# Kernel optimization log

Hardware: AMD Instinct MI355X
Metric: run time of the kernel (lower is better)

Reference implementation:

```python
import jax, jax.numpy as jnp
import numpy as np

HIDDEN = 4096


def setup_inputs() -> dict:
    key = jax.random.key(0)
    k1, k2 = jax.random.split(key)
    hidden_states = jax.random.normal(k1, (8, 2048, HIDDEN), dtype=jnp.float32)
    # gate_proj ~ N(0, 0.02^2), shape (2*hidden, hidden)
    gate_proj = 0.02 * jax.random.normal(k2, (2 * HIDDEN, HIDDEN), dtype=jnp.float32)
    return {"hidden_states": hidden_states, "gate_proj": gate_proj, "world_size": 8}


def reference(hidden_states, gate_proj, world_size):
    h = gate_proj.shape[1]
    view = hidden_states.reshape(-1, h)                 # [N, h]
    mm = jnp.einsum("nh,oh->no", view, gate_proj)      # [N, 2h]  (x @ W.T)
    n, o = mm.shape
    # reduce-scatter over dim 0 with world_size ranks: sum the per-rank chunks
    out = mm.reshape(world_size, n // world_size, o).sum(axis=0)  # [N/W, 2h]
    return out
```

## Files before the change

kernel.cpp:

```cpp
#include <hip/hip_runtime.h>
#include <hip/hip_bf16.h>


#define HID   4096
#define SEQ   2048
#define WORLD 8
#define OUTD  8192

typedef __bf16 bf16x8 __attribute__((ext_vector_type(8)));
typedef short  s16x8  __attribute__((ext_vector_type(8)));
typedef float  f32x4  __attribute__((ext_vector_type(4)));

typedef const __attribute__((address_space(1))) void* gas1_ptr;
typedef __attribute__((address_space(3))) void*       las3_ptr;

static __device__ __forceinline__ unsigned short f2bf(float f) {
    union { float f; unsigned u; } v; v.f = f;
    unsigned u = v.u;
    u += 0x7fffu + ((u >> 16) & 1u);
    return (unsigned short)(u >> 16);
}

#define RED_BLOCKS  2048
#define CONV_BLOCKS 4096
__global__ void prep_kernel(const float* __restrict__ hs,
                            const float* __restrict__ w,
                            unsigned short* __restrict__ xb,
                            unsigned short* __restrict__ wb) {
    if (blockIdx.x < RED_BLOCKS) {
        const int total4 = SEQ * HID / 4;
        const float4* h4 = (const float4*)hs;
        ushort4* o4 = (ushort4*)xb;
        for (int i = blockIdx.x * blockDim.x + threadIdx.x; i < total4;
             i += RED_BLOCKS * blockDim.x) {
            float4 s = h4[i];
            #pragma unroll
            for (int ww = 1; ww < WORLD; ++ww) {
                float4 t = h4[i + ww * total4];
                s.x += t.x; s.y += t.y; s.z += t.z; s.w += t.w;
            }
            ushort4 o;
            o.x = f2bf(s.x); o.y = f2bf(s.y); o.z = f2bf(s.z); o.w = f2bf(s.w);
            o4[i] = o;
        }
    } else {
        const int total4 = OUTD * HID / 4;
        const float4* w4 = (const float4*)w;
        ushort4* o4 = (ushort4*)wb;
        for (int i = (blockIdx.x - RED_BLOCKS) * blockDim.x + threadIdx.x;
             i < total4; i += CONV_BLOCKS * blockDim.x) {
            float4 s = w4[i];
            ushort4 o;
            o.x = f2bf(s.x); o.y = f2bf(s.y); o.z = f2bf(s.z); o.w = f2bf(s.w);
            o4[i] = o;
        }
    }
}


#define BM 256
#define BN 256
#define BK 64
#define KSTEPS (HID / BK)

__global__ __launch_bounds__(512, 2)
void gemm_bt_kernel(const unsigned short* __restrict__ A,
                    const unsigned short* __restrict__ B,
                    float* __restrict__ C) {
    __shared__ __align__(16) unsigned short lsA[2][BM * BK];
    __shared__ __align__(16) unsigned short lsB[2][BN * BK];

    const int tid  = threadIdx.x;
    const int lane = tid & 63;
    const int wave = tid >> 6;
    const int wm   = wave >> 2;
    const int wn   = wave & 3;

    const int bid   = blockIdx.x;
    const int xcd   = bid & 7;
    const int local = bid >> 3;
    const int bm = (xcd >> 2) * 4 + (local >> 3);
    const int bn = (xcd & 3) * 8 + (local & 7);

    const int subrow = lane >> 3;
    const int slot   = lane & 7;
    const int scol   = (slot ^ subrow) * 8;
    const unsigned short* aBase =
        A + (size_t)(bm * BM + wave * 8 + subrow) * HID + scol;
    const unsigned short* bBase =
        B + (size_t)(bn * BN + wave * 8 + subrow) * HID + scol;
    const int ldsW = wave * 8 * BK;

#define ST_A(buf, ktv, l) __builtin_amdgcn_global_load_lds(                     \
        (gas1_ptr)(aBase + (size_t)(ktv) * BK + (size_t)(l) * 64 * HID),        \
        (las3_ptr)(&lsA[buf][(l) * 64 * BK + ldsW]), 16, 0, 0)
#define ST_B(buf, ktv, l) __builtin_amdgcn_global_load_lds(                     \
        (gas1_ptr)(bBase + (size_t)(ktv) * BK + (size_t)(l) * 64 * HID),        \
        (las3_ptr)(&lsB[buf][(l) * 64 * BK + ldsW]), 16, 0, 0)
#define STG_A(buf, ktv, h) do { ST_A(buf, ktv, 2*(h)); ST_A(buf, ktv, 2*(h)+1); } while (0)
#define STG_B(buf, ktv, h) do { ST_B(buf, ktv, 2*(h)); ST_B(buf, ktv, 2*(h)+1); } while (0)

    const int fr    = lane & 15;
    const int fq    = lane >> 4;
    const int axor  = fr & 7;
    const int koff0 = ((0 + fq) ^ axor) * 8;
    const int koff1 = ((4 + fq) ^ axor) * 8;
    const int aRowB = (wm * 128 + fr) * BK;
    const int bRowB = (wn * 64 + fr) * BK;

#define RD_A(dst, P, mm, koff) dst = __builtin_bit_cast(bf16x8,                 \
        *(const s16x8*)&lsA[P][aRowB + (mm) * 16 * BK + (koff)])
#define RD_B(dst, P, nn, koff) dst = __builtin_bit_cast(bf16x8,                 \
        *(const s16x8*)&lsB[P][bRowB + (nn) * 16 * BK + (koff)])

#define BARRIER() __builtin_amdgcn_s_barrier()
#define LGKM0()   asm volatile("s_waitcnt lgkmcnt(0)" ::: "memory")
#define VMC8()    asm volatile("s_waitcnt vmcnt(8)" ::: "memory")
#define VMC0()    asm volatile("s_waitcnt vmcnt(0)" ::: "memory")
#define PRIO1()   __builtin_amdgcn_s_setprio(1)
#define PRIO0()   __builtin_amdgcn_s_setprio(0)

#define MFMA16(VAx, mb)                                                          \
    PRIO1();                                                                     \
    _Pragma("unroll")                                                            \
    for (int s = 0; s < 2; ++s)                                                  \
        _Pragma("unroll")                                                        \
        for (int m = 0; m < 2; ++m)                                              \
            _Pragma("unroll")                                                    \
            for (int n = 0; n < 4; ++n)                                          \
                acc[(mb) + m][n] = __builtin_amdgcn_mfma_f32_16x16x32_bf16(      \
                    VAx[m][s], vb[n][s], acc[(mb) + m][n], 0, 0, 0);             \
    PRIO0()

#define TILE_SECTION(P, Tnext, ST)                                               \
    RD_B(vb[0][0], P, 0, koff0); RD_B(vb[0][1], P, 0, koff1);                    \
    RD_B(vb[1][0], P, 1, koff0); RD_B(vb[1][1], P, 1, koff1);                    \
    RD_B(vb[2][0], P, 2, koff0); RD_B(vb[2][1], P, 2, koff1);                    \
    RD_B(vb[3][0], P, 3, koff0); RD_B(vb[3][1], P, 3, koff1);                    \
    RD_A(va[0][0], P, 0, koff0); RD_A(va[0][1], P, 0, koff1);                    \
    RD_A(va[1][0], P, 1, koff0); RD_A(va[1][1], P, 1, koff1);                    \
    RD_A(vc[0][0], P, 2, koff0); RD_A(vc[0][1], P, 2, koff1);                    \
    RD_A(vc[1][0], P, 3, koff0); RD_A(vc[1][1], P, 3, koff1);                    \
    MFMA16(va, 0);                                                               \
    RD_A(va[0][0], P, 4, koff0); RD_A(va[0][1], P, 4, koff1);                    \
    RD_A(va[1][0], P, 5, koff0); RD_A(va[1][1], P, 5, koff1);                    \
    MFMA16(vc, 2);                                                               \
    RD_A(vc[0][0], P, 6, koff0); RD_A(vc[0][1], P, 6, koff1);                    \
    RD_A(vc[1][0], P, 7, koff0); RD_A(vc[1][1], P, 7, koff1);                    \
    MFMA16(va, 4);                                                               \
    LGKM0();                                                                     \
    BARRIER();                                                                   \
    if (ST) { STG_A(P, Tnext, 0); STG_A(P, Tnext, 1);                            \
              STG_B(P, Tnext, 0); STG_B(P, Tnext, 1); }                          \
    MFMA16(vc, 6);                                                               \
    if (ST) { VMC8(); } else { VMC0(); }                                         \
    BARRIER()

    f32x4 acc[8][4] = {};
    bf16x8 va[2][2], vc[2][2], vb[4][2];

    STG_A(0, 0, 0); STG_A(0, 0, 1); STG_B(0, 0, 0); STG_B(0, 0, 1);
    STG_A(1, 1, 0); STG_A(1, 1, 1); STG_B(1, 1, 0); STG_B(1, 1, 1);
    VMC8();
    BARRIER();

    #pragma unroll 1
    for (int t = 0; t < KSTEPS; t += 2) {
        const bool s2 = (t + 2 < KSTEPS);
        const bool s3 = (t + 3 < KSTEPS);
        TILE_SECTION(0, t + 2, s2);
        TILE_SECTION(1, t + 3, s3);
    }

    const long crow0 = (long)bm * BM + wm * 128 + fq * 4;
    const long ccol0 = (long)bn * BN + wn * 64 + fr;
    #pragma unroll
    for (int m = 0; m < 8; ++m)
        #pragma unroll
        for (int n = 0; n < 4; ++n)
            #pragma unroll
            for (int j = 0; j < 4; ++j)
                C[(crow0 + m * 16 + j) * OUTD + ccol0 + n * 16] = acc[m][n][j];
}

extern "C" void kernel_launch(void* const* d_in, const int* in_sizes, int n_in,
                              void* d_out, int out_size, void* d_ws, size_t ws_size,
                              hipStream_t stream) {
    const float* hs = (const float*)d_in[0];
    const float* w  = (const float*)d_in[1];
    float* out = (float*)d_out;

    unsigned short* xb = (unsigned short*)d_ws;
    unsigned short* wb = xb + (size_t)SEQ * HID;

    hipLaunchKernelGGL(prep_kernel, dim3(RED_BLOCKS + CONV_BLOCKS), dim3(256),
                       0, stream, hs, w, xb, wb);
    hipLaunchKernelGGL(gemm_bt_kernel, dim3((SEQ / BM) * (OUTD / BN)), dim3(512),
                       0, stream, xb, wb, out);
}
```

Measured before the change: 228.2 us.

## Interleave global-to-LDS prefetch chunks across four barrier-separated MFMA phases

Restructures the GEMM main loop into four barrier-separated phases per K-tile, each doing its LDS reads, one chunk of the next-tile global_load_lds prefetch, then an MFMA batch. The prefetch of A and B is spread across the phases, and part of the A tile is issued one tile later into the other buffer, instead of issuing all loads at once after the third MFMA batch. Sched barriers pin the instruction order and the wait is changed to vmcnt(6). The aim is to smooth memory issue and overlap it with compute, at the cost of more barriers per tile and tighter buffer-reuse ordering.

```diff
diff --git a/kernel.cpp b/kernel.cpp
--- a/kernel.cpp
+++ b/kernel.cpp
@@ -115,10 +115,11 @@
 
 #define BARRIER() __builtin_amdgcn_s_barrier()
 #define LGKM0()   asm volatile("s_waitcnt lgkmcnt(0)" ::: "memory")
-#define VMC8()    asm volatile("s_waitcnt vmcnt(8)" ::: "memory")
+#define VMC6()    asm volatile("s_waitcnt vmcnt(6)" ::: "memory")
 #define VMC0()    asm volatile("s_waitcnt vmcnt(0)" ::: "memory")
 #define PRIO1()   __builtin_amdgcn_s_setprio(1)
 #define PRIO0()   __builtin_amdgcn_s_setprio(0)
+#define SB()      __builtin_amdgcn_sched_barrier(0)
 
 #define MFMA16(VAx, mb)                                                          \
     PRIO1();                                                                     \
@@ -132,44 +133,56 @@
                     VAx[m][s], vb[n][s], acc[(mb) + m][n], 0, 0, 0);             \
     PRIO0()
 
-#define TILE_SECTION(P, Tnext, ST)                                               \
+#define TILE_SECTION(P, Q, S, s1, st)                                            \
+                                                              \
+    BARRIER(); SB();                                                             \
     RD_B(vb[0][0], P, 0, koff0); RD_B(vb[0][1], P, 0, koff1);                    \
     RD_B(vb[1][0], P, 1, koff0); RD_B(vb[1][1], P, 1, koff1);                    \
     RD_B(vb[2][0], P, 2, koff0); RD_B(vb[2][1], P, 2, koff1);                    \
     RD_B(vb[3][0], P, 3, koff0); RD_B(vb[3][1], P, 3, koff1);                    \
     RD_A(va[0][0], P, 0, koff0); RD_A(va[0][1], P, 0, koff1);                    \
     RD_A(va[1][0], P, 1, koff0); RD_A(va[1][1], P, 1, koff1);                    \
+    if (s1) STG_A(Q, (S) + 1, 1);                                                \
+    LGKM0(); SB();                                                               \
+    MFMA16(va, 0);                                                               \
+    SB();                                                                        \
+                                                              \
+    BARRIER(); SB();                                                             \
     RD_A(vc[0][0], P, 2, koff0); RD_A(vc[0][1], P, 2, koff1);                    \
     RD_A(vc[1][0], P, 3, koff0); RD_A(vc[1][1], P, 3, koff1);                    \
-    MFMA16(va, 0);                                                               \
     RD_A(va[0][0], P, 4, koff0); RD_A(va[0][1], P, 4, koff1);                    \
     RD_A(va[1][0], P, 5, koff0); RD_A(va[1][1], P, 5, koff1);                    \
+    if (st) STG_B(P, (S) + 2, 0);                                                \
+    LGKM0(); SB();                                                               \
     MFMA16(vc, 2);                                                               \
-    RD_A(vc[0][0], P, 6, koff0); RD_A(vc[0][1], P, 6, koff1);                    \
-    RD_A(vc[1][0], P, 7, koff0); RD_A(vc[1][1], P, 7, koff1);                    \
+    SB();                                                                        \
+                                                              \
+    BARRIER(); SB();                                                             \
+    RD_A(vd[0][0], P, 6, koff0); RD_A(vd[0][1], P, 6, koff1);                    \
+    RD_A(vd[1][0], P, 7, koff0); RD_A(vd[1][1], P, 7, koff1);                    \
+    if (st) STG_B(P, (S) + 2, 1);                                                \
+    LGKM0(); SB();                                                               \
     MFMA16(va, 4);                                                               \
-    LGKM0();                                                                     \
-    BARRIER();                                                                   \
-    if (ST) { STG_A(P, Tnext, 0); STG_A(P, Tnext, 1);                            \
-              STG_B(P, Tnext, 0); STG_B(P, Tnext, 1); }                          \
-    MFMA16(vc, 6);                                                               \
-    if (ST) { VMC8(); } else { VMC0(); }                                         \
-    BARRIER()
+    SB();                                                                        \
+                                                              \
+    BARRIER(); SB();                                                             \
+    if (st) STG_A(P, (S) + 2, 0);                                                \
+    MFMA16(vd, 6);                                                               \
+    if (st) { VMC6(); } else { VMC0(); }                                         \
+    SB()
 
     f32x4 acc[8][4] = {};
-    bf16x8 va[2][2], vc[2][2], vb[4][2];
-
-    STG_A(0, 0, 0); STG_A(0, 0, 1); STG_B(0, 0, 0); STG_B(0, 0, 1);
-    STG_A(1, 1, 0); STG_A(1, 1, 1); STG_B(1, 1, 0); STG_B(1, 1, 1);
-    VMC8();
-    BARRIER();
+    bf16x8 va[2][2], vc[2][2], vd[2][2], vb[4][2];
+
+    STG_B(0, 0, 0); STG_B(0, 0, 1); STG_A(0, 0, 0); STG_A(0, 0, 1);
+    STG_B(1, 1, 0); STG_B(1, 1, 1); STG_A(1, 1, 0);
+    VMC6();
 
     #pragma unroll 1
     for (int t = 0; t < KSTEPS; t += 2) {
-        const bool s2 = (t + 2 < KSTEPS);
-        const bool s3 = (t + 3 < KSTEPS);
-        TILE_SECTION(0, t + 2, s2);
-        TILE_SECTION(1, t + 3, s3);
+        const bool g1 = (t + 1 < KSTEPS), g2 = (t + 2 < KSTEPS), g3 = (t + 3 < KSTEPS);
+        TILE_SECTION(0, 1, t,     g1, g2);
+        TILE_SECTION(1, 0, t + 1, g2, g3);
     }
 
     const long crow0 = (long)bm * BM + wm * 128 + fq * 4;
```

Result: faster. 220.4 us, median of 4 (-3.4%).

## Shrink GEMM tile to 128x128 and load B fragments straight from global

Applied to the files above, without the earlier changes.

Changes the GEMM block tile from 256x256 with 8 waves to 128x128 with 4 waves, and occupancy from 2 to 3 blocks. Only the A tile is staged through LDS with direct global-to-LDS loads. B fragments are now read from global memory straight into registers and prefetched one k-step ahead. Dropping the B LDS buffer and its barriers cuts LDS use and traffic, at the cost of less data reuse per block and duplicated B reads across waves, which now rely on the caches.

```diff
diff --git a/kernel.cpp b/kernel.cpp
--- a/kernel.cpp
+++ b/kernel.cpp
@@ -58,124 +58,116 @@
 }
 
 
-#define BM 256
-#define BN 256
+#define BM 128
+#define BN 128
 #define BK 64
 #define KSTEPS (HID / BK)
 
-__global__ __launch_bounds__(512, 2)
+__global__ __launch_bounds__(256, 3)
 void gemm_bt_kernel(const unsigned short* __restrict__ A,
                     const unsigned short* __restrict__ B,
                     float* __restrict__ C) {
     __shared__ __align__(16) unsigned short lsA[2][BM * BK];
-    __shared__ __align__(16) unsigned short lsB[2][BN * BK];
 
     const int tid  = threadIdx.x;
     const int lane = tid & 63;
     const int wave = tid >> 6;
-    const int wm   = wave >> 2;
-    const int wn   = wave & 3;
+    const int wm   = wave >> 1;
+    const int wn   = wave & 1;
 
     const int bid   = blockIdx.x;
     const int xcd   = bid & 7;
     const int local = bid >> 3;
-    const int bm = (xcd >> 2) * 4 + (local >> 3);
-    const int bn = (xcd & 3) * 8 + (local & 7);
+    const int bm = (xcd >> 2) * 8 + (local >> 4);
+    const int bn = (xcd & 3) * 16 + (local & 15);
 
     const int subrow = lane >> 3;
     const int slot   = lane & 7;
     const int scol   = (slot ^ subrow) * 8;
     const unsigned short* aBase =
         A + (size_t)(bm * BM + wave * 8 + subrow) * HID + scol;
-    const unsigned short* bBase =
-        B + (size_t)(bn * BN + wave * 8 + subrow) * HID + scol;
     const int ldsW = wave * 8 * BK;
 
 #define ST_A(buf, ktv, l) __builtin_amdgcn_global_load_lds(                     \
-        (gas1_ptr)(aBase + (size_t)(ktv) * BK + (size_t)(l) * 64 * HID),        \
-        (las3_ptr)(&lsA[buf][(l) * 64 * BK + ldsW]), 16, 0, 0)
-#define ST_B(buf, ktv, l) __builtin_amdgcn_global_load_lds(                     \
-        (gas1_ptr)(bBase + (size_t)(ktv) * BK + (size_t)(l) * 64 * HID),        \
-        (las3_ptr)(&lsB[buf][(l) * 64 * BK + ldsW]), 16, 0, 0)
-#define STG_A(buf, ktv, h) do { ST_A(buf, ktv, 2*(h)); ST_A(buf, ktv, 2*(h)+1); } while (0)
-#define STG_B(buf, ktv, h) do { ST_B(buf, ktv, 2*(h)); ST_B(buf, ktv, 2*(h)+1); } while (0)
+        (gas1_ptr)(aBase + (size_t)(ktv) * BK + (size_t)(l) * 32 * HID),        \
+        (las3_ptr)(&lsA[buf][(l) * 32 * BK + ldsW]), 16, 0, 0)
+#define STG_A4(buf, ktv) do { ST_A(buf, ktv, 0); ST_A(buf, ktv, 1);             \
+                              ST_A(buf, ktv, 2); ST_A(buf, ktv, 3); } while (0)
 
     const int fr    = lane & 15;
     const int fq    = lane >> 4;
     const int axor  = fr & 7;
     const int koff0 = ((0 + fq) ^ axor) * 8;
     const int koff1 = ((4 + fq) ^ axor) * 8;
-    const int aRowB = (wm * 128 + fr) * BK;
-    const int bRowB = (wn * 64 + fr) * BK;
+    const int aRowB = (wm * 64 + fr) * BK;
 
 #define RD_A(dst, P, mm, koff) dst = __builtin_bit_cast(bf16x8,                 \
         *(const s16x8*)&lsA[P][aRowB + (mm) * 16 * BK + (koff)])
-#define RD_B(dst, P, nn, koff) dst = __builtin_bit_cast(bf16x8,                 \
-        *(const s16x8*)&lsB[P][bRowB + (nn) * 16 * BK + (koff)])
+
+    const unsigned short* b0 =
+        B + (size_t)(bn * BN + wn * 64 + fr) * HID + fq * 8;
+    const unsigned short* b1 = b0 + (size_t)16 * HID;
+    const unsigned short* b2 = b0 + (size_t)32 * HID;
+    const unsigned short* b3 = b0 + (size_t)48 * HID;
+
+#define BC8(p) __builtin_bit_cast(bf16x8, *(const s16x8*)(p))
+#define LOADB() do {                                                            \
+    vb[0][0] = BC8(b0); vb[0][1] = BC8(b0 + 32);                                \
+    vb[1][0] = BC8(b1); vb[1][1] = BC8(b1 + 32);                                \
+    vb[2][0] = BC8(b2); vb[2][1] = BC8(b2 + 32);                                \
+    vb[3][0] = BC8(b3); vb[3][1] = BC8(b3 + 32);                                \
+    b0 += BK; b1 += BK; b2 += BK; b3 += BK; } while (0)
 
 #define BARRIER() __builtin_amdgcn_s_barrier()
-#define LGKM0()   asm volatile("s_waitcnt lgkmcnt(0)" ::: "memory")
 #define VMC8()    asm volatile("s_waitcnt vmcnt(8)" ::: "memory")
-#define VMC0()    asm volatile("s_waitcnt vmcnt(0)" ::: "memory")
 #define PRIO1()   __builtin_amdgcn_s_setprio(1)
 #define PRIO0()   __builtin_amdgcn_s_setprio(0)
+#define SB()      __builtin_amdgcn_sched_barrier(0)
 
-#define MFMA16(VAx, mb)                                                          \
-    PRIO1();                                                                     \
+#define CLUSTER(m)                                                               \
     _Pragma("unroll")                                                            \
     for (int s = 0; s < 2; ++s)                                                  \
         _Pragma("unroll")                                                        \
-        for (int m = 0; m < 2; ++m)                                              \
-            _Pragma("unroll")                                                    \
-            for (int n = 0; n < 4; ++n)                                          \
-                acc[(mb) + m][n] = __builtin_amdgcn_mfma_f32_16x16x32_bf16(      \
-                    VAx[m][s], vb[n][s], acc[(mb) + m][n], 0, 0, 0);             \
-    PRIO0()
+        for (int n = 0; n < 4; ++n)                                              \
+            acc[m][n] = __builtin_amdgcn_mfma_f32_16x16x32_bf16(                 \
+                va[m][s], vb[n][s], acc[m][n], 0, 0, 0)
 
-#define TILE_SECTION(P, Tnext, ST)                                               \
-    RD_B(vb[0][0], P, 0, koff0); RD_B(vb[0][1], P, 0, koff1);                    \
-    RD_B(vb[1][0], P, 1, koff0); RD_B(vb[1][1], P, 1, koff1);                    \
-    RD_B(vb[2][0], P, 2, koff0); RD_B(vb[2][1], P, 2, koff1);                    \
-    RD_B(vb[3][0], P, 3, koff0); RD_B(vb[3][1], P, 3, koff1);                    \
+#define SECTION(P, TT, HN)                                                       \
+    BARRIER(); SB();                                                             \
+    if (HN) { STG_A4((P) ^ 1, (TT) + 1); }                                       \
+    SB();                                                                        \
     RD_A(va[0][0], P, 0, koff0); RD_A(va[0][1], P, 0, koff1);                    \
     RD_A(va[1][0], P, 1, koff0); RD_A(va[1][1], P, 1, koff1);                    \
-    RD_A(vc[0][0], P, 2, koff0); RD_A(vc[0][1], P, 2, koff1);                    \
-    RD_A(vc[1][0], P, 3, koff0); RD_A(vc[1][1], P, 3, koff1);                    \
-    MFMA16(va, 0);                                                               \
-    RD_A(va[0][0], P, 4, koff0); RD_A(va[0][1], P, 4, koff1);                    \
-    RD_A(va[1][0], P, 5, koff0); RD_A(va[1][1], P, 5, koff1);                    \
-    MFMA16(vc, 2);                                                               \
-    RD_A(vc[0][0], P, 6, koff0); RD_A(vc[0][1], P, 6, koff1);                    \
-    RD_A(vc[1][0], P, 7, koff0); RD_A(vc[1][1], P, 7, koff1);                    \
-    MFMA16(va, 4);                                                               \
-    LGKM0();                                                                     \
-    BARRIER();                                                                   \
-    if (ST) { STG_A(P, Tnext, 0); STG_A(P, Tnext, 1);                            \
-              STG_B(P, Tnext, 0); STG_B(P, Tnext, 1); }                          \
-    MFMA16(vc, 6);                                                               \
-    if (ST) { VMC8(); } else { VMC0(); }                                         \
-    BARRIER()
+    RD_A(va[2][0], P, 2, koff0); RD_A(va[2][1], P, 2, koff1);                    \
+    RD_A(va[3][0], P, 3, koff0); RD_A(va[3][1], P, 3, koff1);                    \
+    PRIO1();                                                                     \
+    CLUSTER(0); CLUSTER(1); CLUSTER(2); CLUSTER(3);                              \
+    PRIO0(); SB();                                                               \
+    if (HN) { LOADB(); }                                                         \
+    SB();                                                                        \
+    if (HN) { VMC8(); }                                                          \
+    SB()
 
-    f32x4 acc[8][4] = {};
-    bf16x8 va[2][2], vc[2][2], vb[4][2];
+    f32x4 acc[4][4] = {};
+    bf16x8 va[4][2], vb[4][2];
 
-    STG_A(0, 0, 0); STG_A(0, 0, 1); STG_B(0, 0, 0); STG_B(0, 0, 1);
-    STG_A(1, 1, 0); STG_A(1, 1, 1); STG_B(1, 1, 0); STG_B(1, 1, 1);
+    STG_A4(0, 0);
+    SB();
+    LOADB();
+    SB();
     VMC8();
-    BARRIER();
+    SB();
 
     #pragma unroll 1
     for (int t = 0; t < KSTEPS; t += 2) {
-        const bool s2 = (t + 2 < KSTEPS);
-        const bool s3 = (t + 3 < KSTEPS);
-        TILE_SECTION(0, t + 2, s2);
-        TILE_SECTION(1, t + 3, s3);
+        SECTION(0, t, true);
+        SECTION(1, t + 1, (t + 2 < KSTEPS));
     }
 
-    const long crow0 = (long)bm * BM + wm * 128 + fq * 4;
+    const long crow0 = (long)bm * BM + wm * 64 + fq * 4;
     const long ccol0 = (long)bn * BN + wn * 64 + fr;
     #pragma unroll
-    for (int m = 0; m < 8; ++m)
+    for (int m = 0; m < 4; ++m)
         #pragma unroll
         for (int n = 0; n < 4; ++n)
             #pragma unroll
@@ -195,6 +187,6 @@
 
     hipLaunchKernelGGL(prep_kernel, dim3(RED_BLOCKS + CONV_BLOCKS), dim3(256),
                        0, stream, hs, w, xb, wb);
-    hipLaunchKernelGGL(gemm_bt_kernel, dim3((SEQ / BM) * (OUTD / BN)), dim3(512),
+    hipLaunchKernelGGL(gemm_bt_kernel, dim3((SEQ / BM) * (OUTD / BN)), dim3(256),
                        0, stream, xb, wb, out);
 }
```

New measurement: 376.0 us. 64.7% more time.

## Fuse weight fp32-to-bf16 conversion into GEMM B-tile loading via registers

Applied to the files above, without the earlier changes.

Removes the separate weight conversion pass: the GEMM now reads fp32 weights directly into registers, rounds them to bf16 with a cheaper round-half-up pack, and writes them into swizzled LDS, prefetching two k-steps ahead. The A operand keeps async global-to-LDS loads. This drops a full write and re-read of the 64MB bf16 weight copy, but the GEMM now reads twice the B bytes per tile, each B tile is re-read and converted by all 8 row-blocks of output tiles, and register pressure rises with the 8 f32x4 prefetch registers. The pipeline is also restructured to a single barrier per k-step with the LDS reads split into two half-K passes.

```diff
diff --git a/kernel.cpp b/kernel.cpp
--- a/kernel.cpp
+++ b/kernel.cpp
@@ -21,39 +21,28 @@
     return (unsigned short)(u >> 16);
 }
 
-#define RED_BLOCKS  2048
-#define CONV_BLOCKS 4096
-__global__ void prep_kernel(const float* __restrict__ hs,
-                            const float* __restrict__ w,
-                            unsigned short* __restrict__ xb,
-                            unsigned short* __restrict__ wb) {
-    if (blockIdx.x < RED_BLOCKS) {
-        const int total4 = SEQ * HID / 4;
-        const float4* h4 = (const float4*)hs;
-        ushort4* o4 = (ushort4*)xb;
-        for (int i = blockIdx.x * blockDim.x + threadIdx.x; i < total4;
-             i += RED_BLOCKS * blockDim.x) {
-            float4 s = h4[i];
-            #pragma unroll
-            for (int ww = 1; ww < WORLD; ++ww) {
-                float4 t = h4[i + ww * total4];
-                s.x += t.x; s.y += t.y; s.z += t.z; s.w += t.w;
-            }
-            ushort4 o;
-            o.x = f2bf(s.x); o.y = f2bf(s.y); o.z = f2bf(s.z); o.w = f2bf(s.w);
-            o4[i] = o;
+static __device__ __forceinline__ unsigned pack_bf2(float a, float b) {
+    unsigned ua = __builtin_bit_cast(unsigned, a) + 0x8000u;
+    unsigned ub = __builtin_bit_cast(unsigned, b) + 0x8000u;
+    return (ua >> 16) | (ub & 0xffff0000u);
+}
+
+__global__ void reduce_x_kernel(const float* __restrict__ hs,
+                                unsigned short* __restrict__ xb) {
+    const int total4 = SEQ * HID / 4;
+    const float4* h4 = (const float4*)hs;
+    ushort4* o4 = (ushort4*)xb;
+    for (int i = blockIdx.x * blockDim.x + threadIdx.x; i < total4;
+         i += gridDim.x * blockDim.x) {
+        float4 s = h4[i];
+        #pragma unroll
+        for (int w = 1; w < WORLD; ++w) {
+            float4 t = h4[i + w * total4];
+            s.x += t.x; s.y += t.y; s.z += t.z; s.w += t.w;
         }
-    } else {
-        const int total4 = OUTD * HID / 4;
-        const float4* w4 = (const float4*)w;
-        ushort4* o4 = (ushort4*)wb;
-        for (int i = (blockIdx.x - RED_BLOCKS) * blockDim.x + threadIdx.x;
-             i < total4; i += CONV_BLOCKS * blockDim.x) {
-            float4 s = w4[i];
-            ushort4 o;
-            o.x = f2bf(s.x); o.y = f2bf(s.y); o.z = f2bf(s.z); o.w = f2bf(s.w);
-            o4[i] = o;
-        }
+        ushort4 o;
+        o.x = f2bf(s.x); o.y = f2bf(s.y); o.z = f2bf(s.z); o.w = f2bf(s.w);
+        o4[i] = o;
     }
 }
 
@@ -65,7 +54,7 @@
 
 __global__ __launch_bounds__(512, 2)
 void gemm_bt_kernel(const unsigned short* __restrict__ A,
-                    const unsigned short* __restrict__ B,
+                    const float* __restrict__ W,
                     float* __restrict__ C) {
     __shared__ __align__(16) unsigned short lsA[2][BM * BK];
     __shared__ __align__(16) unsigned short lsB[2][BN * BK];
@@ -87,18 +76,33 @@
     const int scol   = (slot ^ subrow) * 8;
     const unsigned short* aBase =
         A + (size_t)(bm * BM + wave * 8 + subrow) * HID + scol;
-    const unsigned short* bBase =
-        B + (size_t)(bn * BN + wave * 8 + subrow) * HID + scol;
     const int ldsW = wave * 8 * BK;
 
 #define ST_A(buf, ktv, l) __builtin_amdgcn_global_load_lds(                     \
         (gas1_ptr)(aBase + (size_t)(ktv) * BK + (size_t)(l) * 64 * HID),        \
         (las3_ptr)(&lsA[buf][(l) * 64 * BK + ldsW]), 16, 0, 0)
-#define ST_B(buf, ktv, l) __builtin_amdgcn_global_load_lds(                     \
-        (gas1_ptr)(bBase + (size_t)(ktv) * BK + (size_t)(l) * 64 * HID),        \
-        (las3_ptr)(&lsB[buf][(l) * 64 * BK + ldsW]), 16, 0, 0)
-#define STG_A(buf, ktv, h) do { ST_A(buf, ktv, 2*(h)); ST_A(buf, ktv, 2*(h)+1); } while (0)
-#define STG_B(buf, ktv, h) do { ST_B(buf, ktv, 2*(h)); ST_B(buf, ktv, 2*(h)+1); } while (0)
+#define STG_A4(buf, ktv) do { ST_A(buf, ktv, 0); ST_A(buf, ktv, 1);             \
+                              ST_A(buf, ktv, 2); ST_A(buf, ktv, 3); } while (0)
+
+    const int wrow = wave * 32 + (lane >> 1);
+    const int wxor = (lane >> 1) & 7;
+    const float* wBase =
+        W + (size_t)(bn * BN + wrow) * HID + (lane & 1) * 32;
+
+#define LOADB(T) do { _Pragma("unroll")                                         \
+    for (int j = 0; j < 8; ++j)                                                 \
+        breg[j] = *(const f32x4*)(wBase + (size_t)(T) * BK + j * 4); } while (0)
+
+#define WRITE_B(Q) do { _Pragma("unroll")                                       \
+    for (int j = 0; j < 4; ++j) {                                               \
+        int4 wv;                                                                \
+        wv.x = (int)pack_bf2(breg[2*j].x,   breg[2*j].y);                       \
+        wv.y = (int)pack_bf2(breg[2*j].z,   breg[2*j].w);                       \
+        wv.z = (int)pack_bf2(breg[2*j+1].x, breg[2*j+1].y);                     \
+        wv.w = (int)pack_bf2(breg[2*j+1].z, breg[2*j+1].w);                     \
+        *(int4*)&lsB[Q][wrow * BK +                                             \
+            (((((lane & 1) * 4) + j) ^ wxor) * 8)] = wv;                        \
+    } } while (0)
 
     const int fr    = lane & 15;
     const int fq    = lane >> 4;
@@ -120,56 +124,62 @@
 #define PRIO1()   __builtin_amdgcn_s_setprio(1)
 #define PRIO0()   __builtin_amdgcn_s_setprio(0)
 
-#define MFMA16(VAx, mb)                                                          \
+#define MFMA8(VA, mb)                                                            \
     PRIO1();                                                                     \
     _Pragma("unroll")                                                            \
-    for (int s = 0; s < 2; ++s)                                                  \
+    for (int m = 0; m < 2; ++m)                                                  \
         _Pragma("unroll")                                                        \
-        for (int m = 0; m < 2; ++m)                                              \
-            _Pragma("unroll")                                                    \
-            for (int n = 0; n < 4; ++n)                                          \
-                acc[(mb) + m][n] = __builtin_amdgcn_mfma_f32_16x16x32_bf16(      \
-                    VAx[m][s], vb[n][s], acc[(mb) + m][n], 0, 0, 0);             \
+        for (int n = 0; n < 4; ++n)                                              \
+            acc[(mb) + m][n] = __builtin_amdgcn_mfma_f32_16x16x32_bf16(          \
+                VA[m], vb[n], acc[(mb) + m][n], 0, 0, 0);                        \
     PRIO0()
 
-#define TILE_SECTION(P, Tnext, ST)                                               \
-    RD_B(vb[0][0], P, 0, koff0); RD_B(vb[0][1], P, 0, koff1);                    \
-    RD_B(vb[1][0], P, 1, koff0); RD_B(vb[1][1], P, 1, koff1);                    \
-    RD_B(vb[2][0], P, 2, koff0); RD_B(vb[2][1], P, 2, koff1);                    \
-    RD_B(vb[3][0], P, 3, koff0); RD_B(vb[3][1], P, 3, koff1);                    \
-    RD_A(va[0][0], P, 0, koff0); RD_A(va[0][1], P, 0, koff1);                    \
-    RD_A(va[1][0], P, 1, koff0); RD_A(va[1][1], P, 1, koff1);                    \
-    RD_A(vc[0][0], P, 2, koff0); RD_A(vc[0][1], P, 2, koff1);                    \
-    RD_A(vc[1][0], P, 3, koff0); RD_A(vc[1][1], P, 3, koff1);                    \
-    MFMA16(va, 0);                                                               \
-    RD_A(va[0][0], P, 4, koff0); RD_A(va[0][1], P, 4, koff1);                    \
-    RD_A(va[1][0], P, 5, koff0); RD_A(va[1][1], P, 5, koff1);                    \
-    MFMA16(vc, 2);                                                               \
-    RD_A(vc[0][0], P, 6, koff0); RD_A(vc[0][1], P, 6, koff1);                    \
-    RD_A(vc[1][0], P, 7, koff0); RD_A(vc[1][1], P, 7, koff1);                    \
-    MFMA16(va, 4);                                                               \
-    LGKM0();                                                                     \
+#define TILE(P, T, HAS1, HAS2)                                                   \
     BARRIER();                                                                   \
-    if (ST) { STG_A(P, Tnext, 0); STG_A(P, Tnext, 1);                            \
-              STG_B(P, Tnext, 0); STG_B(P, Tnext, 1); }                          \
-    MFMA16(vc, 6);                                                               \
-    if (ST) { VMC8(); } else { VMC0(); }                                         \
-    BARRIER()
+    if (HAS1) { WRITE_B((P) ^ 1); STG_A4((P) ^ 1, (T) + 1); }                    \
+    if (HAS2) { LOADB((T) + 2); }                                                \
+                                                      \
+    RD_B(vb[0], P, 0, koff0); RD_B(vb[1], P, 1, koff0);                          \
+    RD_B(vb[2], P, 2, koff0); RD_B(vb[3], P, 3, koff0);                          \
+    RD_A(va[0], P, 0, koff0); RD_A(va[1], P, 1, koff0);                          \
+    MFMA8(va, 0);                                                                \
+    RD_A(vc[0], P, 2, koff0); RD_A(vc[1], P, 3, koff0);                          \
+    MFMA8(vc, 2);                                                                \
+    RD_A(va[0], P, 4, koff0); RD_A(va[1], P, 5, koff0);                          \
+    MFMA8(va, 4);                                                                \
+    RD_A(vc[0], P, 6, koff0); RD_A(vc[1], P, 7, koff0);                          \
+    MFMA8(vc, 6);                                                                \
+                                                      \
+    RD_B(vb[0], P, 0, koff1); RD_B(vb[1], P, 1, koff1);                          \
+    RD_B(vb[2], P, 2, koff1); RD_B(vb[3], P, 3, koff1);                          \
+    RD_A(va[0], P, 0, koff1); RD_A(va[1], P, 1, koff1);                          \
+    MFMA8(va, 0);                                                                \
+    RD_A(vc[0], P, 2, koff1); RD_A(vc[1], P, 3, koff1);                          \
+    MFMA8(vc, 2);                                                                \
+    RD_A(va[0], P, 4, koff1); RD_A(va[1], P, 5, koff1);                          \
+    MFMA8(va, 4);                                                                \
+    RD_A(vc[0], P, 6, koff1); RD_A(vc[1], P, 7, koff1);                          \
+    LGKM0();                    \
+    MFMA8(vc, 6);                                                                \
+    if ((HAS1) && (HAS2)) { VMC8(); }      \
+    else if (HAS1)        { VMC0(); }
 
     f32x4 acc[8][4] = {};
-    bf16x8 va[2][2], vc[2][2], vb[4][2];
-
-    STG_A(0, 0, 0); STG_A(0, 0, 1); STG_B(0, 0, 0); STG_B(0, 0, 1);
-    STG_A(1, 1, 0); STG_A(1, 1, 1); STG_B(1, 1, 0); STG_B(1, 1, 1);
-    VMC8();
-    BARRIER();
+    bf16x8 va[2], vc[2], vb[4];
+    f32x4 breg[8];
+
+    STG_A4(0, 0);
+    LOADB(0);
+    WRITE_B(0);
+    LOADB(1);
+    LGKM0();
 
     #pragma unroll 1
     for (int t = 0; t < KSTEPS; t += 2) {
-        const bool s2 = (t + 2 < KSTEPS);
-        const bool s3 = (t + 3 < KSTEPS);
-        TILE_SECTION(0, t + 2, s2);
-        TILE_SECTION(1, t + 3, s3);
+        const bool g2 = (t + 2 < KSTEPS);
+        const bool g3 = (t + 3 < KSTEPS);
+        TILE(0, t,     true, g2);
+        TILE(1, t + 1, g2,   g3);
     }
 
     const long crow0 = (long)bm * BM + wm * 128 + fq * 4;
@@ -191,10 +201,8 @@
     float* out = (float*)d_out;
 
     unsigned short* xb = (unsigned short*)d_ws;
-    unsigned short* wb = xb + (size_t)SEQ * HID;
-
-    hipLaunchKernelGGL(prep_kernel, dim3(RED_BLOCKS + CONV_BLOCKS), dim3(256),
-                       0, stream, hs, w, xb, wb);
+
+    hipLaunchKernelGGL(reduce_x_kernel, dim3(2048), dim3(256), 0, stream, hs, xb);
     hipLaunchKernelGGL(gemm_bt_kernel, dim3((SEQ / BM) * (OUTD / BN)), dim3(512),
-                       0, stream, xb, wb, out);
-}
+                       0, stream, xb, w, out);
+}
```

Measured after the change: 273.9 us. 1.2x slower.
